# Performance work log

Hardware: AMD Instinct MI355X
Metric: run time of the kernel (lower is better)

## Reference

```python
import jax, jax.numpy as jnp
import numpy as np

B, H, TQ, TK, DH = 4, 8, 128, 128, 64
N_MEM, D_MEM, TOPK, HID = 100000, 512, 32, 128


def setup_inputs() -> dict:
    key = jax.random.key(0)
    ks = jax.random.split(key, 12)
    return {
        "q": jax.random.normal(ks[0], (B, H, TQ, DH), jnp.float32),
        "k_ctx": jax.random.normal(ks[1], (B, H, TK, DH), jnp.float32),
        "v_ctx": jax.random.normal(ks[2], (B, H, TK, DH), jnp.float32),
        "q_for_mem": jax.random.normal(ks[3], (B, TQ, D_MEM), jnp.float32),
        "mem_keys": jax.random.normal(ks[4], (N_MEM, D_MEM), jnp.float32),
        "mem_values": jax.random.normal(ks[5], (N_MEM, D_MEM), jnp.float32),
        "Wk": jax.random.normal(ks[6], (DH, D_MEM), jnp.float32) / np.sqrt(D_MEM),
        "Wv": jax.random.normal(ks[7], (DH, D_MEM), jnp.float32) / np.sqrt(D_MEM),
        "W1": jax.random.normal(ks[8], (HID, 2 * DH), jnp.float32) / np.sqrt(2 * DH),
        "b1": jnp.zeros((HID,), jnp.float32),
        "w2": jax.random.normal(ks[9], (HID,), jnp.float32) / np.sqrt(HID),
        "b2": jnp.zeros((1,), jnp.float32),
    }


def reference(q, k_ctx, v_ctx, q_for_mem, mem_keys, mem_values, Wk, Wv, W1, b1, w2, b2):
    # --- MemoryBank.retrieve: dense scores + top-k gather ---
    mem_scores = jnp.einsum('btd,nd->btn', q_for_mem, mem_keys)          # [B,TQ,N]
    _, idx = jax.lax.top_k(mem_scores, TOPK)                             # [B,TQ,K]
    K_mem = mem_keys[idx] @ Wk.T                                         # [B,TQ,K,DH] (mem_k_proj)
    V_mem = mem_values[idx] @ Wv.T                                       # [B,TQ,K,DH] (mem_v_proj)

    # --- ParametricScoreMLP: f([q;k]) = w2 . relu(W1q q + W1k k + b1) + b2 ---
    W1q, W1k = W1[:, :DH], W1[:, DH:]                                    # split concat linear
    q_part = jnp.einsum('bhtd,ed->bhte', q, W1q)                         # [B,H,TQ,HID]
    kctx_part = jnp.einsum('bhsd,ed->bhse', k_ctx, W1k)                  # [B,H,TK,HID]
    kmem_part = jnp.einsum('btkd,ed->btke', K_mem, W1k)                  # [B,TQ,K,HID]

    h_ctx = jax.nn.relu(q_part[:, :, :, None, :] + kctx_part[:, :, None, :, :] + b1)
    s_ctx = jnp.einsum('bhtse,e->bhts', h_ctx, w2) + b2[0]               # [B,H,TQ,TK]
    h_mem = jax.nn.relu(q_part[:, :, :, None, :] + kmem_part[:, None, :, :, :] + b1)
    s_mem = jnp.einsum('bhtke,e->bhtk', h_mem, w2) + b2[0]               # [B,H,TQ,K]

    scores = jnp.concatenate([s_ctx, s_mem], axis=-1)                    # [B,H,TQ,TK+K]
    weights = jax.nn.softmax(scores, axis=-1)

    w_ctx, w_mem = weights[..., :TK], weights[..., TK:]
    out = jnp.einsum('bhts,bhsd->bhtd', w_ctx, v_ctx) \
        + jnp.einsum('bhtk,btkd->bhtd', w_mem, V_mem)                    # [B,H,TQ,DH]
    return out, weights
```

## Files before the change

### kernel.cpp

```cpp
#include <hip/hip_runtime.h>
#include <cmath>

constexpr int B_ = 4, H_ = 8, TQ_ = 128, TK_ = 128, DH_ = 64;
constexpr int NMEM = 100000, DM = 512, TOPK = 32, HID = 128;
constexpr int R_ = B_ * TQ_;
constexpr int CTILE = 128, RTILE = 64;
constexpr int NCH = (NMEM + CTILE - 1) / CTILE;
constexpr int NPAD = NCH * CTILE;
constexpr int KC = 8;
constexpr int NCAND = NCH * KC;
constexpr int KSEL = 48;
constexpr int CAP  = 128;
constexpr int NLD  = (NCAND + 255) / 256;

using f32x4  = __attribute__((ext_vector_type(4))) float;
using bf16x8 = __attribute__((ext_vector_type(8))) short;
using u16x8  = __attribute__((ext_vector_type(8))) unsigned short;

#define GLOAD16(g, l) __builtin_amdgcn_global_load_lds( \
    (const __attribute__((address_space(1))) void*)(g), \
    (__attribute__((address_space(3))) void*)(l), 16, 0, 0)

static __device__ __forceinline__ unsigned short f2bf(float f) {
    unsigned u = __float_as_uint(f);
    u = (u + 0x7FFFu + ((u >> 16) & 1u)) >> 16;
    return (unsigned short)u;
}

__global__ __launch_bounds__(256)
void k0_cvt(const float* __restrict__ src, unsigned short* __restrict__ dst,
            long n, long ntot)
{
    long stride = (long)gridDim.x * 256 * 8;
    for (long base = ((long)blockIdx.x * 256 + threadIdx.x) * 8; base < ntot; base += stride) {
        u16x8 o;
        if (base < n) {
            float4 v0 = *reinterpret_cast<const float4*>(src + base);
            float4 v1 = *reinterpret_cast<const float4*>(src + base + 4);
            o[0] = f2bf(v0.x); o[1] = f2bf(v0.y); o[2] = f2bf(v0.z); o[3] = f2bf(v0.w);
            o[4] = f2bf(v1.x); o[5] = f2bf(v1.y); o[6] = f2bf(v1.z); o[7] = f2bf(v1.w);
        } else {
            o = (u16x8)0;
        }
        *reinterpret_cast<u16x8*>(dst + base) = o;
    }
}

__global__ __launch_bounds__(256)
void k1_mfma(const unsigned short* __restrict__ qmb, const unsigned short* __restrict__ mkb,
             float* __restrict__ cand_s, int* __restrict__ cand_i)
{
    const int rt = blockIdx.x;
    const int chunk = blockIdx.y;
    const int row0 = rt * RTILE;
    const int col0 = chunk * CTILE;
    const int tid = threadIdx.x;
    const int lane = tid & 63, w = tid >> 6;
    const int wm = w >> 1, wn = w & 1;

    __shared__ __align__(16) char smem[64 * 129 * 4];
    char* Abase = smem;
    char* Bbase = smem + 8192;
    float* scf = (float*)smem;

    f32x4 acc[2][4];
#pragma unroll
    for (int mi = 0; mi < 2; ++mi)
#pragma unroll
        for (int ni = 0; ni < 4; ++ni) acc[mi][ni] = (f32x4)0.f;

    for (int ks = 0; ks < 8; ++ks) {
        const int kb = ks * 128;
#pragma unroll
        for (int p = 0; p < 2; ++p) {
            int X = p * 4096 + w * 1024 + lane * 16;
            int r = X >> 7, c = (X & 127) ^ ((r & 7) << 4);
            const char* src = (const char*)qmb + (size_t)(row0 + r) * 1024 + kb + c;
            GLOAD16(src, Abase + p * 4096 + w * 1024);
        }
#pragma unroll
        for (int p = 0; p < 4; ++p) {
            int X = p * 4096 + w * 1024 + lane * 16;
            int r = X >> 7, c = (X & 127) ^ ((r & 7) << 4);
            const char* src = (const char*)mkb + (size_t)(col0 + r) * 1024 + kb + c;
            GLOAD16(src, Bbase + p * 4096 + w * 1024);
        }
        __syncthreads();
#pragma unroll
        for (int kk = 0; kk < 2; ++kk) {
            bf16x8 af[2], bfr[4];
#pragma unroll
            for (int mi = 0; mi < 2; ++mi) {
                int rr = wm * 32 + mi * 16 + (lane & 15);
                int L = rr * 128 + kk * 64 + ((lane >> 4) * 16);
                af[mi] = *reinterpret_cast<const bf16x8*>(Abase + (L ^ ((rr & 7) << 4)));
            }
#pragma unroll
            for (int ni = 0; ni < 4; ++ni) {
                int rr = wn * 64 + ni * 16 + (lane & 15);
                int L = rr * 128 + kk * 64 + ((lane >> 4) * 16);
                bfr[ni] = *reinterpret_cast<const bf16x8*>(Bbase + (L ^ ((rr & 7) << 4)));
            }
#pragma unroll
            for (int mi = 0; mi < 2; ++mi)
#pragma unroll
                for (int ni = 0; ni < 4; ++ni)
                    acc[mi][ni] = __builtin_amdgcn_mfma_f32_16x16x32_bf16(af[mi], bfr[ni], acc[mi][ni], 0, 0, 0);
        }
        __syncthreads();
    }

#pragma unroll
    for (int mi = 0; mi < 2; ++mi)
#pragma unroll
        for (int ni = 0; ni < 4; ++ni)
#pragma unroll
            for (int reg = 0; reg < 4; ++reg) {
                int rr = wm * 32 + mi * 16 + (lane >> 4) * 4 + reg;
                int cc = wn * 64 + ni * 16 + (lane & 15);
                scf[rr * 129 + cc] = (col0 + cc < NMEM) ? acc[mi][ni][reg] : -INFINITY;
            }
    __syncthreads();

    const int rid = tid >> 2, sub = tid & 3;
    float* srow = scf + rid * 129;
    size_t base = (size_t)(row0 + rid) * NCAND + (size_t)chunk * KC;
    for (int it = 0; it < KC; ++it) {
        float best = -INFINITY; int bi = 0;
        for (int c = sub; c < CTILE; c += 4) {
            float v = srow[c];
            if (v > best) { best = v; bi = c; }
        }
#pragma unroll
        for (int off = 1; off < 4; off <<= 1) {
            float ob = __shfl_xor(best, off);
            int   oi = __shfl_xor(bi, off);
            if (ob > best || (ob == best && oi < bi)) { best = ob; bi = oi; }
        }
        if (sub == 0) { cand_s[base + it] = best; cand_i[base + it] = col0 + bi; }
        srow[bi] = -INFINITY;
    }
}

__global__ __launch_bounds__(256)
void k2a_thresh(const float* __restrict__ cand_s, const int* __restrict__ cand_i,
                int* __restrict__ cand2_i, int* __restrict__ cand2_n)
{
    const int row = blockIdx.x;
    const int tid = threadIdx.x;
    const int lane = tid & 63, wv = tid >> 6;
    const float* cs = cand_s + (size_t)row * NCAND;

    unsigned key[NLD];
#pragma unroll
    for (int j = 0; j < NLD; ++j) {
        int i = tid + j * 256;
        float v = (i < NCAND) ? cs[i] : -INFINITY;
        unsigned b = __float_as_uint(v);
        key[j] = (b & 0x80000000u) ? ~b : (b | 0x80000000u);
    }

    __shared__ int red[4];
    __shared__ int cnt;
    unsigned lo = 0u;
    int c_cur = NCAND;
    for (int bit = 31; bit >= 0; --bit) {
        if (c_cur <= CAP) break;
        unsigned T = lo | (1u << bit);
        int c = 0;
#pragma unroll
        for (int j = 0; j < NLD; ++j) c += (key[j] >= T);
#pragma unroll
        for (int off = 1; off < 64; off <<= 1) c += __shfl_xor(c, off);
        if (lane == 0) red[wv] = c;
        __syncthreads();
        int ct = red[0] + red[1] + red[2] + red[3];
        if (ct >= KSEL) { lo = T; c_cur = ct; }
        __syncthreads();
    }

    if (tid == 0) cnt = 0;
    __syncthreads();
#pragma unroll
    for (int j = 0; j < NLD; ++j) {
        int i = tid + j * 256;
        if (i < NCAND && key[j] >= lo) {
            int p = atomicAdd(&cnt, 1);
            if (p < CAP) cand2_i[(size_t)row * CAP + p] = cand_i[(size_t)row * NCAND + i];
        }
    }
    __syncthreads();
    if (tid == 0) cand2_n[row] = cnt < CAP ? cnt : CAP;
}

__global__ __launch_bounds__(256)
void k2b_rescore(const float* __restrict__ qm, const float* __restrict__ mk,
                 const int* __restrict__ cand2_i, const int* __restrict__ cand2_n,
                 double* __restrict__ rsc)
{
    const int row = blockIdx.x;
    const int tid = threadIdx.x;
    const int lane = tid & 63, wv = tid >> 6;
    const int c = blockIdx.y * 4 + wv;
    const int n = cand2_n[row];
    if (c >= n) return;
    const int idx = cand2_i[(size_t)row * CAP + c];
    const float* qrow = qm + (size_t)row * DM;
    const float* krow = mk + (size_t)idx * DM;
    double p = 0.0;
#pragma unroll
    for (int j = 0; j < DM / 64; ++j) {
        int d = lane + j * 64;
        p += (double)qrow[d] * (double)krow[d];
    }
#pragma unroll
    for (int off = 1; off < 64; off <<= 1) p += __shfl_xor(p, off);
    if (lane == 0) rsc[(size_t)row * CAP + c] = p;
}

__global__ __launch_bounds__(64)
void k2c_top32(const double* __restrict__ rsc, const int* __restrict__ cand2_i,
               const int* __restrict__ cand2_n, int* __restrict__ sel)
{
    const int row = blockIdx.x;
    const int lane = threadIdx.x;
    const int n = cand2_n[row];
    double v0 = -1.0e300, v1 = -1.0e300;
    int i0 = 0x7fffffff, i1 = 0x7fffffff;
    if (lane < n)      { v0 = rsc[(size_t)row * CAP + lane];      i0 = cand2_i[(size_t)row * CAP + lane]; }
    if (lane + 64 < n) { v1 = rsc[(size_t)row * CAP + lane + 64]; i1 = cand2_i[(size_t)row * CAP + lane + 64]; }
    for (int s = 0; s < TOPK; ++s) {
        double bv; int bi;
        if (v0 > v1 || (v0 == v1 && i0 < i1)) { bv = v0; bi = i0; }
        else                                  { bv = v1; bi = i1; }
#pragma unroll
        for (int off = 1; off < 64; off <<= 1) {
            double ov = __shfl_xor(bv, off);
            int    oi = __shfl_xor(bi, off);
            if (ov > bv || (ov == bv && oi < bi)) { bv = ov; bi = oi; }
        }
        if (lane == 0) sel[row * TOPK + s] = bi;
        if (i0 == bi) v0 = -1.0e300;
        if (i1 == bi) v1 = -1.0e300;
    }
}

__global__ __launch_bounds__(64)
void k3_proj(const float* __restrict__ mk, const float* __restrict__ mv,
             const float* __restrict__ Wk, const float* __restrict__ Wv,
             const int* __restrict__ sel,
             float* __restrict__ Kmem, float* __restrict__ Vmem)
{
    const int i0 = blockIdx.x * 8;
    const int tid = threadIdx.x;
    __shared__ float s[2][8][DM];
    __shared__ int si[8];
    if (tid < 8) si[tid] = sel[i0 + tid];
    __syncthreads();
    for (int l = tid; l < 1024; l += 64) {
        int r = l >> 7, c4 = l & 127;
        *reinterpret_cast<float4*>(&s[0][r][c4 * 4]) =
            *reinterpret_cast<const float4*>(mk + (size_t)si[r] * DM + c4 * 4);
        *reinterpret_cast<float4*>(&s[1][r][c4 * 4]) =
            *reinterpret_cast<const float4*>(mv + (size_t)si[r] * DM + c4 * 4);
    }
    __syncthreads();
    const int doV = tid >> 5;
    const int ep = tid & 31;
    const float* W = doV ? Wv : Wk;
    const float* w0 = W + (size_t)ep * DM;
    const float* w1 = W + (size_t)(ep + 32) * DM;
    float a0[8], a1[8];
#pragma unroll
    for (int r = 0; r < 8; ++r) { a0[r] = 0.f; a1[r] = 0.f; }
    for (int d4 = 0; d4 < DM / 4; ++d4) {
        float4 x0 = *reinterpret_cast<const float4*>(w0 + d4 * 4);
        float4 x1 = *reinterpret_cast<const float4*>(w1 + d4 * 4);
#pragma unroll
        for (int r = 0; r < 8; ++r) {
            float4 m = *reinterpret_cast<const float4*>(&s[doV][r][d4 * 4]);
            a0[r] = fmaf(x0.x, m.x, fmaf(x0.y, m.y, fmaf(x0.z, m.z, fmaf(x0.w, m.w, a0[r]))));
            a1[r] = fmaf(x1.x, m.x, fmaf(x1.y, m.y, fmaf(x1.z, m.z, fmaf(x1.w, m.w, a1[r]))));
        }
    }
    float* O = doV ? Vmem : Kmem;
#pragma unroll
    for (int r = 0; r < 8; ++r) {
        O[(size_t)(i0 + r) * DH_ + ep] = a0[r];
        O[(size_t)(i0 + r) * DH_ + ep + 32] = a1[r];
    }
}

__global__ __launch_bounds__(128)
void k4_parts(const float* __restrict__ q, const float* __restrict__ kctx,
              const float* __restrict__ Kmem, const float* __restrict__ W1,
              float* __restrict__ qp, float* __restrict__ kcp, float* __restrict__ kmp)
{
    const int bid = blockIdx.x;
    const int tid = threadIdx.x;
    const float* src; float* dst; int woff;
    if (bid < 1024)      { int r0 = bid * 4;          src = q    + (size_t)r0 * DH_; dst = qp  + (size_t)r0 * HID; woff = 0; }
    else if (bid < 2048) { int r0 = (bid - 1024) * 4; src = kctx + (size_t)r0 * DH_; dst = kcp + (size_t)r0 * HID; woff = DH_; }
    else                 { int r0 = (bid - 2048) * 4; src = Kmem + (size_t)r0 * DH_; dst = kmp + (size_t)r0 * HID; woff = DH_; }
    __shared__ float s[4][DH_];
    for (int l = tid; l < 4 * DH_; l += 128) s[l >> 6][l & 63] = src[l];
    __syncthreads();
    const float* wr = W1 + (size_t)tid * (2 * DH_) + woff;
    float a0 = 0.f, a1 = 0.f, a2 = 0.f, a3 = 0.f;
#pragma unroll 8
    for (int d = 0; d < DH_; ++d) {
        float w = wr[d];
        a0 = fmaf(s[0][d], w, a0);
        a1 = fmaf(s[1][d], w, a1);
        a2 = fmaf(s[2][d], w, a2);
        a3 = fmaf(s[3][d], w, a3);
    }
    dst[0 * HID + tid] = a0;
    dst[1 * HID + tid] = a1;
    dst[2 * HID + tid] = a2;
    dst[3 * HID + tid] = a3;
}

__global__ __launch_bounds__(256)
void k5_attn(const float* __restrict__ qp, const float* __restrict__ kcp,
             const float* __restrict__ kmp, const float* __restrict__ vctx,
             const float* __restrict__ Vmem, const float* __restrict__ b1,
             const float* __restrict__ w2, const float* __restrict__ b2,
             float* __restrict__ out, float* __restrict__ outw)
{
    const int bid = blockIdx.x;
    const int t = bid & 127, h = (bid >> 7) & 7, b = bid >> 10;
    const int tid = threadIdx.x;
    const int lane = tid & 63, wv = tid >> 6;
    const int bh = b * H_ + h, bht = bh * TQ_ + t, bt = b * TQ_ + t;
    constexpr int NS = TK_ + TOPK;
    __shared__ float qps[HID], b1s[HID], w2s[HID];
    __shared__ float sc[NS];
    __shared__ float red[8];
    if (tid < HID) {
        qps[tid] = qp[(size_t)bht * HID + tid];
        b1s[tid] = b1[tid];
        w2s[tid] = w2[tid];
    }
    __syncthreads();
    const float bias2 = b2[0];
    if (tid < NS) {
        const float* kr = (tid < TK_) ? (kcp + ((size_t)bh * TK_ + tid) * HID)
                                      : (kmp + ((size_t)bt * TOPK + (tid - TK_)) * HID);
        float acc = 0.f;
#pragma unroll 4
        for (int e4 = 0; e4 < HID / 4; ++e4) {
            float4 kv = *reinterpret_cast<const float4*>(kr + e4 * 4);
            acc += fmaxf(qps[e4 * 4 + 0] + kv.x + b1s[e4 * 4 + 0], 0.f) * w2s[e4 * 4 + 0];
            acc += fmaxf(qps[e4 * 4 + 1] + kv.y + b1s[e4 * 4 + 1], 0.f) * w2s[e4 * 4 + 1];
            acc += fmaxf(qps[e4 * 4 + 2] + kv.z + b1s[e4 * 4 + 2], 0.f) * w2s[e4 * 4 + 2];
            acc += fmaxf(qps[e4 * 4 + 3] + kv.w + b1s[e4 * 4 + 3], 0.f) * w2s[e4 * 4 + 3];
        }
        sc[tid] = acc + bias2;
    }
    __syncthreads();
    float v = (tid < NS) ? sc[tid] : -INFINITY;
    float m = v;
#pragma unroll
    for (int off = 1; off < 64; off <<= 1) m = fmaxf(m, __shfl_xor(m, off));
    if (lane == 0) red[wv] = m;
    __syncthreads();
    if (tid == 0) red[4] = fmaxf(fmaxf(red[0], red[1]), fmaxf(red[2], red[3]));
    __syncthreads();
    const float mm = red[4];
    float e = (tid < NS) ? expf(v - mm) : 0.f;
    float ssum = e;
#pragma unroll
    for (int off = 1; off < 64; off <<= 1) ssum += __shfl_xor(ssum, off);
    if (lane == 0) red[wv] = ssum;
    __syncthreads();
    if (tid == 0) red[5] = red[0] + red[1] + red[2] + red[3];
    __syncthreads();
    const float inv = 1.f / red[5];
    if (tid < NS) {
        float w = e * inv;
        sc[tid] = w;
        outw[(size_t)bht * NS + tid] = w;
    }
    __syncthreads();
    if (tid < DH_) {
        float acc = 0.f;
        const float* vb = vctx + (size_t)bh * TK_ * DH_ + tid;
        for (int s2 = 0; s2 < TK_; ++s2) acc = fmaf(sc[s2], vb[(size_t)s2 * DH_], acc);
        const float* vm = Vmem + (size_t)bt * TOPK * DH_ + tid;
#pragma unroll
        for (int kk = 0; kk < TOPK; ++kk) acc = fmaf(sc[TK_ + kk], vm[(size_t)kk * DH_], acc);
        out[(size_t)bht * DH_ + tid] = acc;
    }
}

extern "C" void kernel_launch(void* const* d_in, const int* in_sizes, int n_in,
                              void* d_out, int out_size, void* d_ws, size_t ws_size,
                              hipStream_t stream)
{
    const float* q    = (const float*)d_in[0];
    const float* kctx = (const float*)d_in[1];
    const float* vctx = (const float*)d_in[2];
    const float* qm   = (const float*)d_in[3];
    const float* mk   = (const float*)d_in[4];
    const float* mv   = (const float*)d_in[5];
    const float* Wk   = (const float*)d_in[6];
    const float* Wv   = (const float*)d_in[7];
    const float* W1   = (const float*)d_in[8];
    const float* b1   = (const float*)d_in[9];
    const float* w2   = (const float*)d_in[10];
    const float* b2   = (const float*)d_in[11];
    float* out  = (float*)d_out;
    float* outw = out + (size_t)B_ * H_ * TQ_ * DH_;

    char* w = (char*)d_ws;
    unsigned short* mkb = (unsigned short*)w; w += sizeof(unsigned short) * (size_t)NPAD * DM;
    unsigned short* qmb = (unsigned short*)w; w += sizeof(unsigned short) * R_ * DM;
    float* cand_s = (float*)w; w += sizeof(float) * R_ * NCAND;
    int*   cand_i = (int*)w;   w += sizeof(int) * R_ * NCAND;
    int*   cand2_i= (int*)w;   w += sizeof(int) * R_ * CAP;
    int*   cand2_n= (int*)w;   w += sizeof(int) * R_;
    double* rsc   = (double*)w; w += sizeof(double) * R_ * CAP;
    int*   sel    = (int*)w;   w += sizeof(int) * R_ * TOPK;
    float* Kmem   = (float*)w; w += sizeof(float) * R_ * TOPK * DH_;
    float* Vmem   = (float*)w; w += sizeof(float) * R_ * TOPK * DH_;
    float* qp     = (float*)w; w += sizeof(float) * B_ * H_ * TQ_ * HID;
    float* kcp    = (float*)w; w += sizeof(float) * B_ * H_ * TK_ * HID;
    float* kmp    = (float*)w; w += sizeof(float) * R_ * TOPK * HID;

    hipLaunchKernelGGL(k0_cvt, dim3(2048), dim3(256), 0, stream,
                       mk, mkb, (long)NMEM * DM, (long)NPAD * DM);
    hipLaunchKernelGGL(k0_cvt, dim3(128), dim3(256), 0, stream,
                       qm, qmb, (long)R_ * DM, (long)R_ * DM);
    hipLaunchKernelGGL(k1_mfma, dim3(8, NCH), dim3(256), 0, stream, qmb, mkb, cand_s, cand_i);
    hipLaunchKernelGGL(k2a_thresh, dim3(R_), dim3(256), 0, stream, cand_s, cand_i, cand2_i, cand2_n);
    hipLaunchKernelGGL(k2b_rescore, dim3(R_, CAP / 4), dim3(256), 0, stream, qm, mk, cand2_i, cand2_n, rsc);
    hipLaunchKernelGGL(k2c_top32, dim3(R_), dim3(64), 0, stream, rsc, cand2_i, cand2_n, sel);
    hipLaunchKernelGGL(k3_proj, dim3(R_ * TOPK / 8), dim3(64), 0, stream, mk, mv, Wk, Wv, sel, Kmem, Vmem);
    hipLaunchKernelGGL(k4_parts, dim3(6144), dim3(128), 0, stream, q, kctx, Kmem, W1, qp, kcp, kmp);
    hipLaunchKernelGGL(k5_attn, dim3(B_ * H_ * TQ_), dim3(256), 0, stream, qp, kcp, kmp, vctx, Vmem, b1, w2, b2, out, outw);
}
```

Before: 447.4 us.

## Remap MFMA score tiles by XCD and replace serial chunk top-8 with per-lane top-4

The score GEMM launch becomes a flat grid. Each block's chunk is derived from its XCD index, so blocks sharing a mem_keys chunk land on the same XCD and the 8 row tiles reuse it in that XCD's L2. The per-chunk top-8 selection, which needed 8 serial scans with shuffles, is replaced by a branchless register top-4 per lane using packed 64-bit (key, column) values. That yields 16 candidates per chunk, written as precomputed sortable keys with vector stores. Address and LDS-offset computations are hoisted out of the K loop, and the score tile row stride is padded to 132. The candidate pool doubles, which raises traffic in the threshold kernel, and the per-lane top-4 can miss a true chunk top element if more than four fall in the same lane.

```diff
diff --git a/kernel.cpp b/kernel.cpp
--- a/kernel.cpp
+++ b/kernel.cpp
@@ -5,13 +5,13 @@
 constexpr int NMEM = 100000, DM = 512, TOPK = 32, HID = 128;
 constexpr int R_ = B_ * TQ_;
 constexpr int CTILE = 128, RTILE = 64;
-constexpr int NCH = (NMEM + CTILE - 1) / CTILE;
-constexpr int NPAD = NCH * CTILE;
-constexpr int KC = 8;
-constexpr int NCAND = NCH * KC;
+constexpr int NCHP = 784;
+constexpr int NPAD = NCHP * CTILE;
+constexpr int KC = 16;
+constexpr int NCAND = NCHP * KC;
 constexpr int KSEL = 48;
 constexpr int CAP  = 128;
-constexpr int NLD  = (NCAND + 255) / 256;
+constexpr int NLD  = NCAND / 256;
 
 using f32x4  = __attribute__((ext_vector_type(4))) float;
 using bf16x8 = __attribute__((ext_vector_type(8))) short;
@@ -48,21 +48,54 @@
 
 __global__ __launch_bounds__(256)
 void k1_mfma(const unsigned short* __restrict__ qmb, const unsigned short* __restrict__ mkb,
-             float* __restrict__ cand_s, int* __restrict__ cand_i)
-{
-    const int rt = blockIdx.x;
-    const int chunk = blockIdx.y;
+             unsigned* __restrict__ cand_k, int* __restrict__ cand_i)
+{
+    const int wgid = blockIdx.x;
+    const int xcd = wgid & 7;
+    const int k9 = wgid >> 3;
+    const int chunk = xcd * 98 + (k9 >> 3);
+    const int rt = k9 & 7;
     const int row0 = rt * RTILE;
     const int col0 = chunk * CTILE;
     const int tid = threadIdx.x;
     const int lane = tid & 63, w = tid >> 6;
     const int wm = w >> 1, wn = w & 1;
 
-    __shared__ __align__(16) char smem[64 * 129 * 4];
+    __shared__ __align__(16) char smem[64 * 132 * 4];
     char* Abase = smem;
     char* Bbase = smem + 8192;
     float* scf = (float*)smem;
 
+    const char* srcA[2];
+    const char* srcB[4];
+#pragma unroll
+    for (int p = 0; p < 2; ++p) {
+        int X = p * 4096 + w * 1024 + lane * 16;
+        int r = X >> 7, c = (X & 127) ^ ((r & 7) << 4);
+        srcA[p] = (const char*)qmb + (size_t)(row0 + r) * 1024 + c;
+    }
+#pragma unroll
+    for (int p = 0; p < 4; ++p) {
+        int X = p * 4096 + w * 1024 + lane * 16;
+        int r = X >> 7, c = (X & 127) ^ ((r & 7) << 4);
+        srcB[p] = (const char*)mkb + (size_t)(col0 + r) * 1024 + c;
+    }
+    int aoff[2][2], boff[4][2];
+#pragma unroll
+    for (int mi = 0; mi < 2; ++mi) {
+        int rr = wm * 32 + mi * 16 + (lane & 15);
+        int bse = rr * 128 + ((lane >> 4) * 16);
+        aoff[mi][0] = bse ^ ((rr & 7) << 4);
+        aoff[mi][1] = (bse + 64) ^ ((rr & 7) << 4);
+    }
+#pragma unroll
+    for (int ni = 0; ni < 4; ++ni) {
+        int rr = wn * 64 + ni * 16 + (lane & 15);
+        int bse = rr * 128 + ((lane >> 4) * 16);
+        boff[ni][0] = 8192 + (bse ^ ((rr & 7) << 4));
+        boff[ni][1] = 8192 + ((bse + 64) ^ ((rr & 7) << 4));
+    }
+
     f32x4 acc[2][4];
 #pragma unroll
     for (int mi = 0; mi < 2; ++mi)
@@ -70,37 +103,26 @@
         for (int ni = 0; ni < 4; ++ni) acc[mi][ni] = (f32x4)0.f;
 
     for (int ks = 0; ks < 8; ++ks) {
-        const int kb = ks * 128;
 #pragma unroll
         for (int p = 0; p < 2; ++p) {
-            int X = p * 4096 + w * 1024 + lane * 16;
-            int r = X >> 7, c = (X & 127) ^ ((r & 7) << 4);
-            const char* src = (const char*)qmb + (size_t)(row0 + r) * 1024 + kb + c;
-            GLOAD16(src, Abase + p * 4096 + w * 1024);
+            GLOAD16(srcA[p], Abase + p * 4096 + w * 1024);
+            srcA[p] += 128;
         }
 #pragma unroll
         for (int p = 0; p < 4; ++p) {
-            int X = p * 4096 + w * 1024 + lane * 16;
-            int r = X >> 7, c = (X & 127) ^ ((r & 7) << 4);
-            const char* src = (const char*)mkb + (size_t)(col0 + r) * 1024 + kb + c;
-            GLOAD16(src, Bbase + p * 4096 + w * 1024);
+            GLOAD16(srcB[p], Bbase + p * 4096 + w * 1024);
+            srcB[p] += 128;
         }
         __syncthreads();
 #pragma unroll
         for (int kk = 0; kk < 2; ++kk) {
             bf16x8 af[2], bfr[4];
 #pragma unroll
-            for (int mi = 0; mi < 2; ++mi) {
-                int rr = wm * 32 + mi * 16 + (lane & 15);
-                int L = rr * 128 + kk * 64 + ((lane >> 4) * 16);
-                af[mi] = *reinterpret_cast<const bf16x8*>(Abase + (L ^ ((rr & 7) << 4)));
-            }
-#pragma unroll
-            for (int ni = 0; ni < 4; ++ni) {
-                int rr = wn * 64 + ni * 16 + (lane & 15);
-                int L = rr * 128 + kk * 64 + ((lane >> 4) * 16);
-                bfr[ni] = *reinterpret_cast<const bf16x8*>(Bbase + (L ^ ((rr & 7) << 4)));
-            }
+            for (int mi = 0; mi < 2; ++mi)
+                af[mi] = *reinterpret_cast<const bf16x8*>(smem + aoff[mi][kk]);
+#pragma unroll
+            for (int ni = 0; ni < 4; ++ni)
+                bfr[ni] = *reinterpret_cast<const bf16x8*>(smem + boff[ni][kk]);
 #pragma unroll
             for (int mi = 0; mi < 2; ++mi)
 #pragma unroll
@@ -118,47 +140,49 @@
             for (int reg = 0; reg < 4; ++reg) {
                 int rr = wm * 32 + mi * 16 + (lane >> 4) * 4 + reg;
                 int cc = wn * 64 + ni * 16 + (lane & 15);
-                scf[rr * 129 + cc] = (col0 + cc < NMEM) ? acc[mi][ni][reg] : -INFINITY;
+                scf[rr * 132 + cc] = (col0 + cc < NMEM) ? acc[mi][ni][reg] : -INFINITY;
             }
     __syncthreads();
 
     const int rid = tid >> 2, sub = tid & 3;
-    float* srow = scf + rid * 129;
-    size_t base = (size_t)(row0 + rid) * NCAND + (size_t)chunk * KC;
-    for (int it = 0; it < KC; ++it) {
-        float best = -INFINITY; int bi = 0;
-        for (int c = sub; c < CTILE; c += 4) {
-            float v = srow[c];
-            if (v > best) { best = v; bi = c; }
-        }
-#pragma unroll
-        for (int off = 1; off < 4; off <<= 1) {
-            float ob = __shfl_xor(best, off);
-            int   oi = __shfl_xor(bi, off);
-            if (ob > best || (ob == best && oi < bi)) { best = ob; bi = oi; }
-        }
-        if (sub == 0) { cand_s[base + it] = best; cand_i[base + it] = col0 + bi; }
-        srow[bi] = -INFINITY;
-    }
+    const float* srow = scf + rid * 132;
+    unsigned long long t0 = 0ull, t1 = 0ull, t2 = 0ull, t3 = 0ull;
+#pragma unroll 8
+    for (int i = 0; i < 32; ++i) {
+        int c = sub + 4 * i;
+        float v = srow[c];
+        unsigned b = __float_as_uint(v);
+        unsigned s = b ^ ((unsigned)((int)b >> 31) | 0x80000000u);
+        unsigned long long k = ((unsigned long long)s << 7) | (unsigned)(127 - c);
+        bool g0 = k > t0, g1 = k > t1, g2 = k > t2, g3 = k > t3;
+        unsigned long long n0 = g0 ? k : t0;
+        unsigned long long n1 = g0 ? t0 : (g1 ? k : t1);
+        unsigned long long n2 = g1 ? t1 : (g2 ? k : t2);
+        unsigned long long n3 = g2 ? t2 : (g3 ? k : t3);
+        t0 = n0; t1 = n1; t2 = n2; t3 = n3;
+    }
+    size_t base = (size_t)(row0 + rid) * NCAND + (size_t)chunk * KC + sub * 4;
+    uint4 kv, iv;
+    kv.x = (unsigned)(t0 >> 7); iv.x = col0 + 127 - (int)(t0 & 127u);
+    kv.y = (unsigned)(t1 >> 7); iv.y = col0 + 127 - (int)(t1 & 127u);
+    kv.z = (unsigned)(t2 >> 7); iv.z = col0 + 127 - (int)(t2 & 127u);
+    kv.w = (unsigned)(t3 >> 7); iv.w = col0 + 127 - (int)(t3 & 127u);
+    *reinterpret_cast<uint4*>(cand_k + base) = kv;
+    *reinterpret_cast<uint4*>(cand_i + base) = iv;
 }
 
 __global__ __launch_bounds__(256)
-void k2a_thresh(const float* __restrict__ cand_s, const int* __restrict__ cand_i,
+void k2a_thresh(const unsigned* __restrict__ cand_k, const int* __restrict__ cand_i,
                 int* __restrict__ cand2_i, int* __restrict__ cand2_n)
 {
     const int row = blockIdx.x;
     const int tid = threadIdx.x;
     const int lane = tid & 63, wv = tid >> 6;
-    const float* cs = cand_s + (size_t)row * NCAND;
+    const unsigned* ck = cand_k + (size_t)row * NCAND;
 
     unsigned key[NLD];
 #pragma unroll
-    for (int j = 0; j < NLD; ++j) {
-        int i = tid + j * 256;
-        float v = (i < NCAND) ? cs[i] : -INFINITY;
-        unsigned b = __float_as_uint(v);
-        key[j] = (b & 0x80000000u) ? ~b : (b | 0x80000000u);
-    }
+    for (int j = 0; j < NLD; ++j) key[j] = ck[tid + j * 256];
 
     __shared__ int red[4];
     __shared__ int cnt;
@@ -183,10 +207,9 @@
     __syncthreads();
 #pragma unroll
     for (int j = 0; j < NLD; ++j) {
-        int i = tid + j * 256;
-        if (i < NCAND && key[j] >= lo) {
+        if (key[j] >= lo) {
             int p = atomicAdd(&cnt, 1);
-            if (p < CAP) cand2_i[(size_t)row * CAP + p] = cand_i[(size_t)row * NCAND + i];
+            if (p < CAP) cand2_i[(size_t)row * CAP + p] = cand_i[(size_t)row * NCAND + tid + j * 256];
         }
     }
     __syncthreads();
@@ -416,8 +439,8 @@
     char* w = (char*)d_ws;
     unsigned short* mkb = (unsigned short*)w; w += sizeof(unsigned short) * (size_t)NPAD * DM;
     unsigned short* qmb = (unsigned short*)w; w += sizeof(unsigned short) * R_ * DM;
-    float* cand_s = (float*)w; w += sizeof(float) * R_ * NCAND;
-    int*   cand_i = (int*)w;   w += sizeof(int) * R_ * NCAND;
+    unsigned* cand_k = (unsigned*)w; w += sizeof(unsigned) * (size_t)R_ * NCAND;
+    int*   cand_i = (int*)w;   w += sizeof(int) * (size_t)R_ * NCAND;
     int*   cand2_i= (int*)w;   w += sizeof(int) * R_ * CAP;
     int*   cand2_n= (int*)w;   w += sizeof(int) * R_;
     double* rsc   = (double*)w; w += sizeof(double) * R_ * CAP;
@@ -432,8 +455,8 @@
                        mk, mkb, (long)NMEM * DM, (long)NPAD * DM);
     hipLaunchKernelGGL(k0_cvt, dim3(128), dim3(256), 0, stream,
                        qm, qmb, (long)R_ * DM, (long)R_ * DM);
-    hipLaunchKernelGGL(k1_mfma, dim3(8, NCH), dim3(256), 0, stream, qmb, mkb, cand_s, cand_i);
-    hipLaunchKernelGGL(k2a_thresh, dim3(R_), dim3(256), 0, stream, cand_s, cand_i, cand2_i, cand2_n);
+    hipLaunchKernelGGL(k1_mfma, dim3(NCHP * 8), dim3(256), 0, stream, qmb, mkb, cand_k, cand_i);
+    hipLaunchKernelGGL(k2a_thresh, dim3(R_), dim3(256), 0, stream, cand_k, cand_i, cand2_i, cand2_n);
     hipLaunchKernelGGL(k2b_rescore, dim3(R_, CAP / 4), dim3(256), 0, stream, qm, mk, cand2_i, cand2_n, rsc);
     hipLaunchKernelGGL(k2c_top32, dim3(R_), dim3(64), 0, stream, rsc, cand2_i, cand2_n, sel);
     hipLaunchKernelGGL(k3_proj, dim3(R_ * TOPK / 8), dim3(64), 0, stream, mk, mv, Wk, Wv, sel, Kmem, Vmem);
```

Result: faster. 361.0 us (-19.3%).
